# Kernel tuning notes

Measured on AMD Instinct MI355X. Metric: run time of the kernel, lower is better.

Reference implementation:

```python
import jax, jax.numpy as jnp
import numpy as np

EMBED_DIM = 768
FF_DIM = 3072
NUM_EXPERTS = 8
TOP_K = 2
CAPACITY_FACTOR = 1.25  # training-mode capacity factor
LB_WEIGHT = 0.01
Z_WEIGHT = 0.001


def setup_inputs() -> dict:
    key = jax.random.key(0)
    k0, k1, k2, k3, k4 = jax.random.split(key, 5)
    B, S, D, F, E = 4, 2048, EMBED_DIM, FF_DIM, NUM_EXPERTS
    scale_d = 1.0 / np.sqrt(D)
    scale_f = 1.0 / np.sqrt(F)
    return {
        "x": jax.random.normal(k0, (B, S, D), dtype=jnp.float32),
        # router gate: nn.Linear(D, E, bias=False) -> weight [E, D]
        "w_gate": jax.random.normal(k1, (E, D), dtype=jnp.float32) * scale_d,
        # stacked expert weights, torch Linear layout [out, in]
        "wi_gate": jax.random.normal(k2, (E, F, D), dtype=jnp.float32) * scale_d,
        "wi_up": jax.random.normal(k3, (E, F, D), dtype=jnp.float32) * scale_d,
        "wo": jax.random.normal(k4, (E, D, F), dtype=jnp.float32) * scale_f,
    }


def moe_forward(x, w_gate, wi_gate, wi_up, wo):
    B, S, D = x.shape
    E = w_gate.shape[0]
    K = TOP_K
    T = B * S
    capacity = max(int(T * K / E * CAPACITY_FACTOR), K)

    xf = x.reshape(T, D)
    router_logits = xf @ w_gate.T                        # [T, E]
    router_probs = jax.nn.softmax(router_logits, axis=-1)
    topk_probs, topk_idx = jax.lax.top_k(router_probs, K)  # [T, K]
    topk_probs = topk_probs / topk_probs.sum(axis=-1, keepdims=True)

    # one-hot dispatch mask [T, K, E]
    onehot = (topk_idx[:, :, None] == jnp.arange(E)[None, None, :]).astype(xf.dtype)
    # per-(k, expert) arrival rank of each token (torch truncates first `capacity`
    # tokens in token-index order, independently per k and per expert)
    rank = ((jnp.cumsum(onehot, axis=0) - onehot) * onehot).sum(-1)  # [T, K]
    keep = (rank < capacity).astype(xf.dtype)                        # [T, K]

    # combine weights per (token, expert) [T, E]
    combine = jnp.einsum('tk,tk,tke->te', topk_probs, keep, onehot)

    out = jnp.zeros_like(xf)
    for e in range(E):  # fixed small structural loop over experts
        gate = jax.nn.silu(xf @ wi_gate[e].T)   # [T, F]
        up = xf @ wi_up[e].T                    # [T, F]
        y = (gate * up) @ wo[e].T               # [T, D]
        out = out + y * combine[:, e:e + 1]

    # auxiliary losses
    expert_mask = onehot.sum(axis=1)            # [T, E]
    f = expert_mask.sum(axis=0) / (T * K)
    P = router_probs.mean(axis=0)
    load_balance_loss = E * (f * P).sum()
    z_loss = jnp.mean(jax.nn.logsumexp(router_logits, axis=-1) ** 2)
    aux_loss = LB_WEIGHT * load_balance_loss + Z_WEIGHT * z_loss

    return out.reshape(B, S, D), aux_loss


def reference(x, w_gate, wi_gate, wi_up, wo):
    return moe_forward(x, w_gate, wi_gate, wi_up, wo)
```

## Files before the change

### kernel.cpp

```cpp
#include <hip/hip_runtime.h>

typedef unsigned short u16;
typedef unsigned int u32;
typedef unsigned long long u64;

#define T_TOK 8192
#define DIM 768
#define FF 3072
#define NE 8
#define CAP 2560
#define LSTR 5120

typedef __attribute__((ext_vector_type(8))) short s8v;
typedef __attribute__((ext_vector_type(4))) float f4v;

__device__ __forceinline__ u16 f2bf(float f) {
  union { float f; u32 u; } v; v.f = f;
  u32 r = v.u + 0x7FFFu + ((v.u >> 16) & 1u);
  return (u16)(r >> 16);
}

__device__ __forceinline__ void glds16(const void* g, void* l) {
  __builtin_amdgcn_global_load_lds(
      (const __attribute__((address_space(1))) u32*)g,
      (__attribute__((address_space(3))) u32*)l, 16, 0, 0);
}

#define BARRIER() do { asm volatile("" ::: "memory"); __builtin_amdgcn_s_barrier(); asm volatile("" ::: "memory"); } while (0)
#define WAITV(N) asm volatile("s_waitcnt vmcnt(" #N ")" ::: "memory")
#define WAITL() asm volatile("s_waitcnt lgkmcnt(0)" ::: "memory")
#define PRIO1 __builtin_amdgcn_s_setprio(1)
#define PRIO0 __builtin_amdgcn_s_setprio(0)

__global__ __launch_bounds__(256) void cast3_kernel(
    const float* __restrict__ s0, const float* __restrict__ s1, const float* __restrict__ s2,
    u16* __restrict__ d0, u16* __restrict__ d1, u16* __restrict__ d2, int n8each) {
  int i = blockIdx.x * 256 + threadIdx.x;
  const float* s; u16* d; int j;
  if (i < n8each) { s = s0; d = d0; j = i; }
  else if (i < 2 * n8each) { s = s1; d = d1; j = i - n8each; }
  else { s = s2; d = d2; j = i - 2 * n8each; }
  const float4* s4 = (const float4*)s;
  float4 a = s4[2 * j], b = s4[2 * j + 1];
  uint4 o;
  o.x = (u32)f2bf(a.x) | ((u32)f2bf(a.y) << 16);
  o.y = (u32)f2bf(a.z) | ((u32)f2bf(a.w) << 16);
  o.z = (u32)f2bf(b.x) | ((u32)f2bf(b.y) << 16);
  o.w = (u32)f2bf(b.z) | ((u32)f2bf(b.w) << 16);
  ((uint4*)d)[j] = o;
}

__global__ __launch_bounds__(256) void router_kernel(
    const float* __restrict__ x, const float* __restrict__ wg, u16* __restrict__ xb,
    int* __restrict__ tki, float* __restrict__ tkp,
    float* __restrict__ probs, float* __restrict__ lse2) {
  int lane = threadIdx.x & 63;
  int t = blockIdx.x * 4 + (threadIdx.x >> 6);
  const float* xr = x + (long)t * DIM;
  u16* xw = xb + (long)t * DIM;
  float acc[NE];
#pragma unroll
  for (int e = 0; e < NE; e++) acc[e] = 0.f;
  for (int i = 0; i < DIM / 64; i++) {
    float xv = xr[lane + 64 * i];
    xw[lane + 64 * i] = f2bf(xv);
#pragma unroll
    for (int e = 0; e < NE; e++) acc[e] += xv * wg[e * DIM + lane + 64 * i];
  }
#pragma unroll
  for (int off = 32; off > 0; off >>= 1) {
#pragma unroll
    for (int e = 0; e < NE; e++) acc[e] += __shfl_xor(acc[e], off);
  }
  if (lane == 0) {
    float m = acc[0];
#pragma unroll
    for (int e = 1; e < NE; e++) m = fmaxf(m, acc[e]);
    float p[NE], s = 0.f;
#pragma unroll
    for (int e = 0; e < NE; e++) { p[e] = __expf(acc[e] - m); s += p[e]; }
    float inv = 1.f / s;
    int e0 = 0;
#pragma unroll
    for (int e = 1; e < NE; e++) if (acc[e] > acc[e0]) e0 = e;
    int e1 = (e0 == 0) ? 1 : 0;
#pragma unroll
    for (int e = 0; e < NE; e++) if (e != e0 && acc[e] > acc[e1]) e1 = e;
    float p0 = p[e0] * inv, p1 = p[e1] * inv;
    float rn = 1.f / (p0 + p1);
    tki[2 * t] = e0; tki[2 * t + 1] = e1;
    tkp[2 * t] = p0 * rn; tkp[2 * t + 1] = p1 * rn;
    float4 pa = {p[0] * inv, p[1] * inv, p[2] * inv, p[3] * inv};
    float4 pb = {p[4] * inv, p[5] * inv, p[6] * inv, p[7] * inv};
    ((float4*)(probs + t * 8))[0] = pa;
    ((float4*)(probs + t * 8))[1] = pb;
    float lse = __logf(s) + m;
    lse2[t] = lse * lse;
  }
}

__global__ __launch_bounds__(1024) void reduce_router_kernel(
    const int* __restrict__ tki, const float* __restrict__ probs, const float* __restrict__ lse2,
    int* __restrict__ fcnt, float* __restrict__ psum, float* __restrict__ zsum) {
  int t = blockIdx.x * 1024 + threadIdx.x;
  float4 pa = ((const float4*)(probs + t * 8))[0];
  float4 pb = ((const float4*)(probs + t * 8))[1];
  float p[8] = {pa.x, pa.y, pa.z, pa.w, pb.x, pb.y, pb.z, pb.w};
  float z = lse2[t];
  int e0 = tki[2 * t], e1 = tki[2 * t + 1];
  int fc[8];
#pragma unroll
  for (int e = 0; e < 8; e++) fc[e] = (e0 == e ? 1 : 0) + (e1 == e ? 1 : 0);
#pragma unroll
  for (int off = 32; off > 0; off >>= 1) {
#pragma unroll
    for (int e = 0; e < 8; e++) { p[e] += __shfl_xor(p[e], off); fc[e] += __shfl_xor(fc[e], off); }
    z += __shfl_xor(z, off);
  }
  __shared__ float sp[16][9];
  __shared__ int sf[16][8];
  int wv = threadIdx.x >> 6, lane = threadIdx.x & 63;
  if (lane == 0) {
#pragma unroll
    for (int e = 0; e < 8; e++) { sp[wv][e] = p[e]; sf[wv][e] = fc[e]; }
    sp[wv][8] = z;
  }
  __syncthreads();
  if (threadIdx.x < 9) {
    float s = 0.f;
    for (int w = 0; w < 16; w++) s += sp[w][threadIdx.x];
    if (threadIdx.x < 8) atomicAdd(&psum[threadIdx.x], s);
    else atomicAdd(zsum, s);
  }
  if (threadIdx.x >= 64 && threadIdx.x < 72) {
    int e = threadIdx.x - 64;
    int s = 0;
    for (int w = 0; w < 16; w++) s += sf[w][e];
    atomicAdd(&fcnt[e], s);
  }
}

__global__ __launch_bounds__(1024) void rank_dispatch_kernel(
    const int* __restrict__ tki, const float* __restrict__ tkp,
    int* __restrict__ ltk, float* __restrict__ lw,
    int* __restrict__ counts, int* __restrict__ baserow, int* __restrict__ kflags) {
  __shared__ int wave_cnt[2][16][8];
  __shared__ int base[2][8];
  __shared__ int sc0[8];
  int tid = threadIdx.x, wv = tid >> 6, lane = tid & 63;
  int c0w[8];
#pragma unroll
  for (int e = 0; e < 8; e++) c0w[e] = 0;
  for (int c = 0; c < T_TOK / 1024; c++) {
    int e0 = tki[2 * (c * 1024 + tid)];
#pragma unroll
    for (int e = 0; e < 8; e++) {
      u64 m = __ballot(e0 == e);
      if (lane == 0) c0w[e] += __popcll(m);
    }
  }
  if (lane == 0) {
#pragma unroll
    for (int e = 0; e < 8; e++) wave_cnt[0][wv][e] = c0w[e];
  }
  if (tid < 16) base[tid >> 3][tid & 7] = 0;
  __syncthreads();
  if (tid < 8) {
    int s = 0;
    for (int w = 0; w < 16; w++) s += wave_cnt[0][w][tid];
    sc0[tid] = (s < CAP) ? s : CAP;
  }
  __syncthreads();
  u64 lmask = (lane == 63) ? 0x7FFFFFFFFFFFFFFFull : ((1ull << lane) - 1ull);
  for (int c = 0; c < T_TOK / 1024; c++) {
    int t = c * 1024 + tid;
    int e0 = tki[2 * t], e1 = tki[2 * t + 1];
    float p0 = tkp[2 * t], p1 = tkp[2 * t + 1];
    int pre0 = 0, pre1 = 0;
    for (int e = 0; e < 8; e++) {
      u64 m0 = __ballot(e0 == e);
      if (e0 == e) pre0 = __popcll(m0 & lmask);
      if (lane == 0) wave_cnt[0][wv][e] = __popcll(m0);
      u64 m1 = __ballot(e1 == e);
      if (e1 == e) pre1 = __popcll(m1 & lmask);
      if (lane == 0) wave_cnt[1][wv][e] = __popcll(m1);
    }
    __syncthreads();
    if (tid < 16) {
      int k = tid >> 3, e = tid & 7;
      int run = base[k][e];
      for (int w = 0; w < 16; w++) {
        int v = wave_cnt[k][w][e];
        wave_cnt[k][w][e] = run;
        run += v;
      }
      base[k][e] = run;
    }
    __syncthreads();
    int r0 = wave_cnt[0][wv][e0] + pre0;
    int r1 = wave_cnt[1][wv][e1] + pre1;
    if (r0 < CAP) { ltk[e0 * LSTR + r0] = (t << 1); lw[e0 * LSTR + r0] = p0; }
    if (r1 < CAP) {
      int p = sc0[e1] + r1;
      ltk[e1 * LSTR + p] = (t << 1) | 1; lw[e1 * LSTR + p] = p1;
    }
    kflags[t] = (r0 < CAP ? 1 : 0) | (r1 < CAP ? 2 : 0);
    __syncthreads();
  }
  if (tid == 0) {
    int run = 0;
    for (int e = 0; e < 8; e++) {
      int c1 = base[1][e]; if (c1 > CAP) c1 = CAP;
      int cnt = sc0[e] + c1;
      counts[e] = cnt; baserow[e] = run; run += cnt;
    }
  }
}

#define LOADA(MS, PB) \
  _Pragma("unroll") for (int i_ = 0; i_ < 4; i_++) { \
    const u16* rp_ = (PB) + ((MS) * 64 + i_ * 16 + lrow) * 64; \
    a[i_][0] = *(const s8v*)(rp_ + sx0); \
    a[i_][1] = *(const s8v*)(rp_ + sx1); }
#define LOADB(DST, NS, PB) \
  _Pragma("unroll") for (int j_ = 0; j_ < 2; j_++) { \
    const u16* rp_ = (PB) + (cb + (NS) * 32 + j_ * 16 + lrow) * 64; \
    DST[j_][0] = *(const s8v*)(rp_ + sx0); \
    DST[j_][1] = *(const s8v*)(rp_ + sx1); }
#define QMFMA(MS, NS, BREG) \
  _Pragma("unroll") for (int i_ = 0; i_ < 4; i_++) { \
    _Pragma("unroll") for (int j_ = 0; j_ < 2; j_++) { \
      acc[(MS) * 4 + i_][(NS) * 2 + j_] = __builtin_amdgcn_mfma_f32_16x16x32_bf16( \
          a[i_][0], BREG[j_][0], acc[(MS) * 4 + i_][(NS) * 2 + j_], 0, 0, 0); \
      acc[(MS) * 4 + i_][(NS) * 2 + j_] = __builtin_amdgcn_mfma_f32_16x16x32_bf16( \
          a[i_][1], BREG[j_][1], acc[(MS) * 4 + i_][(NS) * 2 + j_], 0, 0, 0); } }

#define STAGE_A(P, H, KT) do { \
    glds16(gAbase + (offA[H][0] + (u32)((KT) * 64)), aLds + ((P) * 2 + (H)) * 8192 + t8); \
    glds16(gAbase + (offA[H][1] + (u32)((KT) * 64)), aLds + ((P) * 2 + (H)) * 8192 + 4096 + t8); \
  } while (0)
#define STAGE_B(P, H, KT) do { \
    glds16(gBbase + (offB[H][0] + (u32)((KT) * 64)), bLds + ((P) * 2 + (H)) * 8192 + t8); \
    glds16(gBbase + (offB[H][1] + (u32)((KT) * 64)), bLds + ((P) * 2 + (H)) * 8192 + 4096 + t8); \
  } while (0)

#define KTILE(KT, P, NK, WVN) do { \
    const u16* Ap = Awb + (P) * 16384; \
    const u16* Bp = Bwb + (P) * 16384; \
    LOADA(0, Ap); \
    LOADB(b0, 0, Bp); \
    if ((KT) + 1 < (NK)) STAGE_A((P) ^ 1, 1, (KT) + 1); \
    BARRIER(); WAITL(); \
    PRIO1; QMFMA(0, 0, b0); PRIO0; \
    BARRIER(); \
    LOADB(b1, 1, Bp); \
    if ((KT) + 1 < (NK)) STAGE_B((P) ^ 1, 1, (KT) + 1); \
    BARRIER(); WAITL(); \
    PRIO1; QMFMA(0, 1, b1); PRIO0; \
    BARRIER(); \
    LOADA(1, Ap); \
    if ((KT) + 2 < (NK)) STAGE_B(P, 0, (KT) + 2); \
    BARRIER(); WAITL(); \
    PRIO1; QMFMA(1, 1, b1); PRIO0; \
    BARRIER(); \
    if ((KT) + 2 < (NK)) STAGE_A(P, 0, (KT) + 2); \
    if ((KT) < (NK) - 2) { WAITV(4); } else { WAITV(0); } \
    BARRIER(); \
    PRIO1; QMFMA(1, 0, b0); PRIO0; \
    BARRIER(); \
  } while (0)

__global__ __launch_bounds__(512, 2) void gemm1_kernel(
    const u16* __restrict__ xb, const u16* __restrict__ wgb, const u16* __restrict__ wub,
    u16* __restrict__ H, const int* __restrict__ counts, const int* __restrict__ baserow,
    const int* __restrict__ ltk) {
  int id = blockIdx.x;
  int wgi = (id & 7) * 240 + (id >> 3);
  int e = wgi / 240;
  int rem = wgi - e * 240;
  int NT = rem / 10;
  int mt = rem - NT * 10;
  int cnt = counts[e];
  if (mt * 256 >= cnt) return;

  __shared__ u16 A[2][2][128 * 64];
  __shared__ u16 B[2][2][128 * 64];
  __shared__ int toks[256];
  int tid = threadIdx.x;
  if (tid < 256) {
    int r = mt * 256 + tid; if (r > cnt - 1) r = cnt - 1;
    toks[tid] = ltk[e * LSTR + r] >> 1;
  }
  __syncthreads();

  const u16* gAbase = xb;
  const u16* gBbase = wgb;
  u16* aLds = &A[0][0][0];
  u16* bLds = &B[0][0][0];
  int t8 = tid * 8;
  int row0 = tid >> 3, row1 = row0 + 64;
  int lsw = ((tid & 7) ^ (row0 & 7)) * 8;
  u32 offA[2][2], offB[2][2];
#pragma unroll
  for (int h = 0; h < 2; h++) {
    offA[h][0] = (u32)toks[h * 128 + row0] * DIM + lsw;
    offA[h][1] = (u32)toks[h * 128 + row1] * DIM + lsw;
#pragma unroll
    for (int c = 0; c < 2; c++) {
      int rowc = c ? row1 : row0;
      int rr = NT * 256 + h * 128 + rowc;
      int f = ((rr >> 5) << 4) + (rr & 15);
      u32 o = (u32)(e * FF + f) * DIM + lsw;
      if ((rr >> 4) & 1) o += (u32)NE * FF * DIM;
      offB[h][c] = o;
    }
  }

  int lane = tid & 63, wv = tid >> 6;
  int wm = (wv & 1) * 128;
  int wn = (wv >> 1) * 64;
  int lrow = lane & 15, quad = lane >> 4;
  int cb = wn & 64;
  int sx0 = (quad ^ (lrow & 7)) * 8;
  int sx1 = ((quad + 4) ^ (lrow & 7)) * 8;
  const u16* Awb = &A[0][wm >> 7][0];
  const u16* Bwb = &B[0][wn >> 7][0];

  f4v acc[8][4];
#pragma unroll
  for (int i = 0; i < 8; i++)
#pragma unroll
    for (int j = 0; j < 4; j++) acc[i][j] = (f4v){0.f, 0.f, 0.f, 0.f};
  s8v a[4][2], b0[2][2], b1[2][2];

  STAGE_A(0, 0, 0); STAGE_A(0, 1, 0); STAGE_B(0, 0, 0); STAGE_B(0, 1, 0);
  STAGE_B(1, 0, 1); STAGE_A(1, 0, 1);
  WAITV(4);
  BARRIER();

#pragma unroll 1
  for (int kt = 0; kt < 12; kt += 2) {
    KTILE(kt, 0, 12, 4);
    KTILE(kt + 1, 1, 12, 4);
  }

  long hb = (long)baserow[e] + (long)mt * 256;
#pragma unroll
  for (int mi = 0; mi < 8; mi++) {
#pragma unroll
    for (int r4 = 0; r4 < 4; r4++) {
      int m = wm + (mi >> 2) * 64 + (mi & 3) * 16 + quad * 4 + r4;
      if (mt * 256 + m < cnt) {
#pragma unroll
        for (int pr = 0; pr < 2; pr++) {
          float gv = acc[mi][pr * 2][r4], uv = acc[mi][pr * 2 + 1][r4];
          float h = gv / (1.f + __expf(-gv)) * uv;
          H[(hb + m) * FF + NT * 128 + (wn >> 1) + pr * 16 + lrow] = f2bf(h);
        }
      }
    }
  }
}

__global__ __launch_bounds__(512, 2) void gemm2_kernel(
    const u16* __restrict__ Hsrc, const u16* __restrict__ wob,
    float* __restrict__ ybuf, const int* __restrict__ counts, const int* __restrict__ baserow,
    const int* __restrict__ ltk, const float* __restrict__ lw) {
  int id = blockIdx.x;
  int wgi = (id & 7) * 30 + (id >> 3);
  int e = wgi / 30;
  int rem = wgi - e * 30;
  int mt = rem / 3;
  int nt = rem - mt * 3;
  int cnt = counts[e];
  if (mt * 256 >= cnt) return;

  __shared__ u16 A[2][2][128 * 64];
  __shared__ u16 B[2][2][128 * 64];
  __shared__ int stok[256];
  __shared__ float sw[256];
  int tid = threadIdx.x;
  if (tid < 256) {
    int r = mt * 256 + tid; if (r > cnt - 1) r = cnt - 1;
    stok[tid] = ltk[e * LSTR + r];
    sw[tid] = lw[e * LSTR + r];
  }
  __syncthreads();
  int hb0 = baserow[e];

  const u16* gAbase = Hsrc;
  const u16* gBbase = wob;
  u16* aLds = &A[0][0][0];
  u16* bLds = &B[0][0][0];
  int t8 = tid * 8;
  int row0 = tid >> 3, row1 = row0 + 64;
  int lsw = ((tid & 7) ^ (row0 & 7)) * 8;
  u32 offA[2][2], offB[2][2];
#pragma unroll
  for (int h = 0; h < 2; h++) {
#pragma unroll
    for (int c = 0; c < 2; c++) {
      int rowc = c ? row1 : row0;
      int r_ = mt * 256 + h * 128 + rowc; if (r_ > cnt - 1) r_ = cnt - 1;
      offA[h][c] = (u32)(hb0 + r_) * FF + lsw;
      offB[h][c] = (u32)(e * DIM + nt * 256 + h * 128 + rowc) * FF + lsw;
    }
  }

  int lane = tid & 63, wv = tid >> 6;
  int wm = (wv & 1) * 128;
  int wn = (wv >> 1) * 64;
  int lrow = lane & 15, quad = lane >> 4;
  int cb = wn & 64;
  int sx0 = (quad ^ (lrow & 7)) * 8;
  int sx1 = ((quad + 4) ^ (lrow & 7)) * 8;
  const u16* Awb = &A[0][wm >> 7][0];
  const u16* Bwb = &B[0][wn >> 7][0];

  f4v acc[8][4];
#pragma unroll
  for (int i = 0; i < 8; i++)
#pragma unroll
    for (int j = 0; j < 4; j++) acc[i][j] = (f4v){0.f, 0.f, 0.f, 0.f};
  s8v a[4][2], b0[2][2], b1[2][2];

  STAGE_A(0, 0, 0); STAGE_A(0, 1, 0); STAGE_B(0, 0, 0); STAGE_B(0, 1, 0);
  STAGE_B(1, 0, 1); STAGE_A(1, 0, 1);
  WAITV(4);
  BARRIER();

#pragma unroll 1
  for (int kt = 0; kt < 48; kt += 2) {
    KTILE(kt, 0, 48, 4);
    KTILE(kt + 1, 1, 48, 4);
  }

#pragma unroll
  for (int mi = 0; mi < 8; mi++) {
#pragma unroll
    for (int r4 = 0; r4 < 4; r4++) {
      int m = wm + (mi >> 2) * 64 + (mi & 3) * 16 + quad * 4 + r4;
      if (mt * 256 + m < cnt) {
        int entry = stok[m];
        float w = sw[m];
        long ob = (long)entry * DIM + nt * 256 + wn;
#pragma unroll
        for (int jc = 0; jc < 4; jc++)
          ybuf[ob + jc * 16 + lrow] = acc[mi][jc][r4] * w;
      }
    }
  }
}

__global__ __launch_bounds__(256) void combine_kernel(
    const float* __restrict__ ybuf, const int* __restrict__ kflags, float* __restrict__ out) {
  int idx = blockIdx.x * 256 + threadIdx.x;
  int t = idx / (DIM / 4);
  int d4 = idx - t * (DIM / 4);
  int kf = kflags[t];
  float4 r = {0.f, 0.f, 0.f, 0.f};
  if (kf & 1) {
    float4 a = ((const float4*)(ybuf + (long)(2 * t) * DIM))[d4];
    r.x += a.x; r.y += a.y; r.z += a.z; r.w += a.w;
  }
  if (kf & 2) {
    float4 b = ((const float4*)(ybuf + (long)(2 * t + 1) * DIM))[d4];
    r.x += b.x; r.y += b.y; r.z += b.z; r.w += b.w;
  }
  ((float4*)out)[idx] = r;
}

__global__ void aux_kernel(const int* __restrict__ fcnt, const float* __restrict__ psum,
                           const float* __restrict__ zsum, float* __restrict__ outaux) {
  if (threadIdx.x == 0 && blockIdx.x == 0) {
    float lb = 0.f;
    for (int e = 0; e < 8; e++)
      lb += ((float)fcnt[e] / (float)(T_TOK * 2)) * (psum[e] / (float)T_TOK);
    lb *= 8.f;
    float z = zsum[0] / (float)T_TOK;
    outaux[0] = 0.01f * lb + 0.001f * z;
  }
}

extern "C" void kernel_launch(void* const* d_in, const int* in_sizes, int n_in,
                              void* d_out, int out_size, void* d_ws, size_t ws_size,
                              hipStream_t stream) {
  const float* x = (const float*)d_in[0];
  const float* wgate = (const float*)d_in[1];
  const float* wig = (const float*)d_in[2];
  const float* wiu = (const float*)d_in[3];
  const float* wo = (const float*)d_in[4];
  float* out = (float*)d_out;

  char* ws = (char*)d_ws;
  size_t off = 0;
  auto alloc = [&](size_t bytes) {
    void* p = ws + off;
    off += (bytes + 255) & ~(size_t)255;
    return p;
  };
  int* ctrl = (int*)alloc(256);
  u16* xb = (u16*)alloc((size_t)T_TOK * DIM * 2);
  u16* wgb = (u16*)alloc((size_t)NE * FF * DIM * 2);
  u16* wub = (u16*)alloc((size_t)NE * FF * DIM * 2);
  u16* wob = (u16*)alloc((size_t)NE * DIM * FF * 2);
  u16* Hbuf = (u16*)alloc((size_t)(T_TOK * 2 + 256) * FF * 2);
  int* tki = (int*)alloc((size_t)T_TOK * 2 * 4);
  float* tkp = (float*)alloc((size_t)T_TOK * 2 * 4);
  int* ltk = (int*)alloc((size_t)NE * LSTR * 4);
  float* lw = (float*)alloc((size_t)NE * LSTR * 4);
  float* probs = (float*)alloc((size_t)T_TOK * 8 * 4);
  float* lse2 = (float*)alloc((size_t)T_TOK * 4);
  int* kflags = (int*)alloc((size_t)T_TOK * 4);
  float* ybuf = (float*)wgb;

  int* fcnt = ctrl;
  int* counts = ctrl + 8;
  int* baserow = ctrl + 16;
  float* psum = (float*)(ctrl + 24);
  float* zsum = (float*)(ctrl + 32);

  const int n8each = NE * FF * DIM / 8;
  hipMemsetAsync(ctrl, 0, 256, stream);
  cast3_kernel<<<3 * n8each / 256, 256, 0, stream>>>(wig, wiu, wo, wgb, wub, wob, n8each);
  router_kernel<<<T_TOK / 4, 256, 0, stream>>>(x, wgate, xb, tki, tkp, probs, lse2);
  reduce_router_kernel<<<T_TOK / 1024, 1024, 0, stream>>>(tki, probs, lse2, fcnt, psum, zsum);
  rank_dispatch_kernel<<<1, 1024, 0, stream>>>(tki, tkp, ltk, lw, counts, baserow, kflags);
  gemm1_kernel<<<1920, 512, 0, stream>>>(xb, wgb, wub, Hbuf, counts, baserow, ltk);
  gemm2_kernel<<<240, 512, 0, stream>>>(Hbuf, wob, ybuf, counts, baserow, ltk, lw);
  combine_kernel<<<T_TOK * DIM / 4 / 256, 256, 0, stream>>>(ybuf, kflags, out);
  aux_kernel<<<1, 64, 0, stream>>>(fcnt, psum, zsum, out + (size_t)T_TOK * DIM);
}
```

Before: 616.2 us.

## Merge weight cast with router kernel and restructure GEMM k-tile prefetch schedule

Folds the bf16 weight-cast kernel and the router kernel into a single launch, with the block index picking the role, so one launch is saved and the two independent jobs can overlap. In both expert GEMMs, the prefetch of the next k-tiles is moved from a staggered half-tile pattern to staging both halves of A and B two tiles ahead at later points in each k-tile, with the vmcnt wait raised to match. This changes how much global-to-LDS traffic is in flight during the MFMA phases. It risks fewer loads overlapping the early MFMA blocks and a buffer hazard if the staging order is wrong.

After: 626.5 us. No clear change (+1.7%).

```diff
diff --git a/kernel.cpp b/kernel.cpp
--- a/kernel.cpp
+++ b/kernel.cpp
@@ -10,6 +10,7 @@
 #define NE 8
 #define CAP 2560
 #define LSTR 5120
+#define NCAST 27648
 
 typedef __attribute__((ext_vector_type(8))) short s8v;
 typedef __attribute__((ext_vector_type(4))) float f4v;
@@ -32,30 +33,32 @@
 #define PRIO1 __builtin_amdgcn_s_setprio(1)
 #define PRIO0 __builtin_amdgcn_s_setprio(0)
 
-__global__ __launch_bounds__(256) void cast3_kernel(
-    const float* __restrict__ s0, const float* __restrict__ s1, const float* __restrict__ s2,
-    u16* __restrict__ d0, u16* __restrict__ d1, u16* __restrict__ d2, int n8each) {
-  int i = blockIdx.x * 256 + threadIdx.x;
-  const float* s; u16* d; int j;
-  if (i < n8each) { s = s0; d = d0; j = i; }
-  else if (i < 2 * n8each) { s = s1; d = d1; j = i - n8each; }
-  else { s = s2; d = d2; j = i - 2 * n8each; }
-  const float4* s4 = (const float4*)s;
-  float4 a = s4[2 * j], b = s4[2 * j + 1];
-  uint4 o;
-  o.x = (u32)f2bf(a.x) | ((u32)f2bf(a.y) << 16);
-  o.y = (u32)f2bf(a.z) | ((u32)f2bf(a.w) << 16);
-  o.z = (u32)f2bf(b.x) | ((u32)f2bf(b.y) << 16);
-  o.w = (u32)f2bf(b.z) | ((u32)f2bf(b.w) << 16);
-  ((uint4*)d)[j] = o;
-}
-
-__global__ __launch_bounds__(256) void router_kernel(
+__global__ __launch_bounds__(256) void pre_kernel(
+    const float* __restrict__ wig, const float* __restrict__ wiu, const float* __restrict__ wo,
+    u16* __restrict__ wgb, u16* __restrict__ wub, u16* __restrict__ wob, int n8each,
     const float* __restrict__ x, const float* __restrict__ wg, u16* __restrict__ xb,
     int* __restrict__ tki, float* __restrict__ tkp,
     float* __restrict__ probs, float* __restrict__ lse2) {
+  int bid = blockIdx.x;
+  if (bid < NCAST) {
+    int i = bid * 256 + threadIdx.x;
+    const float* s; u16* d; int j;
+    if (i < n8each) { s = wig; d = wgb; j = i; }
+    else if (i < 2 * n8each) { s = wiu; d = wub; j = i - n8each; }
+    else { s = wo; d = wob; j = i - 2 * n8each; }
+    const float4* s4 = (const float4*)s;
+    float4 a = s4[2 * j], b = s4[2 * j + 1];
+    uint4 o;
+    o.x = (u32)f2bf(a.x) | ((u32)f2bf(a.y) << 16);
+    o.y = (u32)f2bf(a.z) | ((u32)f2bf(a.w) << 16);
+    o.z = (u32)f2bf(b.x) | ((u32)f2bf(b.y) << 16);
+    o.w = (u32)f2bf(b.z) | ((u32)f2bf(b.w) << 16);
+    ((uint4*)d)[j] = o;
+    return;
+  }
+  int rb = bid - NCAST;
   int lane = threadIdx.x & 63;
-  int t = blockIdx.x * 4 + (threadIdx.x >> 6);
+  int t = rb * 4 + (threadIdx.x >> 6);
   const float* xr = x + (long)t * DIM;
   u16* xw = xb + (long)t * DIM;
   float acc[NE];
@@ -244,27 +247,25 @@
     glds16(gBbase + (offB[H][1] + (u32)((KT) * 64)), bLds + ((P) * 2 + (H)) * 8192 + 4096 + t8); \
   } while (0)
 
-#define KTILE(KT, P, NK, WVN) do { \
+#define KTILE(KT, P, NK) do { \
     const u16* Ap = Awb + (P) * 16384; \
     const u16* Bp = Bwb + (P) * 16384; \
     LOADA(0, Ap); \
     LOADB(b0, 0, Bp); \
-    if ((KT) + 1 < (NK)) STAGE_A((P) ^ 1, 1, (KT) + 1); \
     BARRIER(); WAITL(); \
     PRIO1; QMFMA(0, 0, b0); PRIO0; \
     BARRIER(); \
     LOADB(b1, 1, Bp); \
-    if ((KT) + 1 < (NK)) STAGE_B((P) ^ 1, 1, (KT) + 1); \
     BARRIER(); WAITL(); \
     PRIO1; QMFMA(0, 1, b1); PRIO0; \
     BARRIER(); \
     LOADA(1, Ap); \
-    if ((KT) + 2 < (NK)) STAGE_B(P, 0, (KT) + 2); \
+    if ((KT) + 2 < (NK)) { STAGE_B(P, 0, (KT) + 2); STAGE_B(P, 1, (KT) + 2); } \
     BARRIER(); WAITL(); \
     PRIO1; QMFMA(1, 1, b1); PRIO0; \
     BARRIER(); \
-    if ((KT) + 2 < (NK)) STAGE_A(P, 0, (KT) + 2); \
-    if ((KT) < (NK) - 2) { WAITV(4); } else { WAITV(0); } \
+    if ((KT) + 2 < (NK)) { STAGE_A(P, 0, (KT) + 2); STAGE_A(P, 1, (KT) + 2); } \
+    if ((KT) < (NK) - 2) { WAITV(8); } else { WAITV(0); } \
     BARRIER(); \
     PRIO1; QMFMA(1, 0, b0); PRIO0; \
     BARRIER(); \
@@ -334,14 +335,14 @@
   s8v a[4][2], b0[2][2], b1[2][2];
 
   STAGE_A(0, 0, 0); STAGE_A(0, 1, 0); STAGE_B(0, 0, 0); STAGE_B(0, 1, 0);
-  STAGE_B(1, 0, 1); STAGE_A(1, 0, 1);
-  WAITV(4);
+  STAGE_A(1, 0, 1); STAGE_A(1, 1, 1); STAGE_B(1, 0, 1); STAGE_B(1, 1, 1);
+  WAITV(8);
   BARRIER();
 
 #pragma unroll 1
   for (int kt = 0; kt < 12; kt += 2) {
-    KTILE(kt, 0, 12, 4);
-    KTILE(kt + 1, 1, 12, 4);
+    KTILE(kt, 0, 12);
+    KTILE(kt + 1, 1, 12);
   }
 
   long hb = (long)baserow[e] + (long)mt * 256;
@@ -425,14 +426,14 @@
   s8v a[4][2], b0[2][2], b1[2][2];
 
   STAGE_A(0, 0, 0); STAGE_A(0, 1, 0); STAGE_B(0, 0, 0); STAGE_B(0, 1, 0);
-  STAGE_B(1, 0, 1); STAGE_A(1, 0, 1);
-  WAITV(4);
+  STAGE_A(1, 0, 1); STAGE_A(1, 1, 1); STAGE_B(1, 0, 1); STAGE_B(1, 1, 1);
+  WAITV(8);
   BARRIER();
 
 #pragma unroll 1
   for (int kt = 0; kt < 48; kt += 2) {
-    KTILE(kt, 0, 48, 4);
-    KTILE(kt + 1, 1, 48, 4);
+    KTILE(kt, 0, 48);
+    KTILE(kt + 1, 1, 48);
   }
 
 #pragma unroll
@@ -522,8 +523,8 @@
 
   const int n8each = NE * FF * DIM / 8;
   hipMemsetAsync(ctrl, 0, 256, stream);
-  cast3_kernel<<<3 * n8each / 256, 256, 0, stream>>>(wig, wiu, wo, wgb, wub, wob, n8each);
-  router_kernel<<<T_TOK / 4, 256, 0, stream>>>(x, wgate, xb, tki, tkp, probs, lse2);
+  pre_kernel<<<NCAST + T_TOK / 4, 256, 0, stream>>>(
+      wig, wiu, wo, wgb, wub, wob, n8each, x, wgate, xb, tki, tkp, probs, lse2);
   reduce_router_kernel<<<T_TOK / 1024, 1024, 0, stream>>>(tki, probs, lse2, fcnt, psum, zsum);
   rank_dispatch_kernel<<<1, 1024, 0, stream>>>(tki, tkp, ltk, lw, counts, baserow, kflags);
   gemm1_kernel<<<1920, 512, 0, stream>>>(xb, wgb, wub, Hbuf, counts, baserow, ltk);
```
